# Kernel optimization log

Hardware: AMD Instinct MI355X
Metric: run time of the kernel (lower is better)

## Reference

```python
import jax, jax.numpy as jnp
import numpy as np

N = 20000       # num_nodes
B = 4           # batch
D = 32          # input_dim
OUT = 64        # output_dim
S = 2           # n_supports
E = 640000      # edges per support (avg degree 32)
MAX_STEP = 3
M = MAX_STEP * S + 1  # num_metrics = 7


def setup_inputs() -> dict:
    key = jax.random.key(0)
    k = jax.random.split(key, 6)
    inputs = jax.random.normal(k[0], (B, N, D), dtype=jnp.float32)
    edge_src = jax.random.randint(k[1], (S, E), 0, N, dtype=jnp.int32)
    edge_dst = jax.random.randint(k[2], (S, E), 0, N, dtype=jnp.int32)
    # ~1/deg scaled values so the diffusion recurrence stays numerically tame
    edge_vals = jax.random.uniform(k[3], (S, E), dtype=jnp.float32) / 32.0
    W = jax.random.normal(k[4], (OUT, D * M), dtype=jnp.float32) * 0.05
    bias = jnp.zeros((OUT,), dtype=jnp.float32)
    return dict(inputs=inputs, edge_vals=edge_vals, W=W, bias=bias,
                edge_src=edge_src, edge_dst=edge_dst)


def _spmm(vals, src, dst, x):
    # y[i] = sum_{edges (i<-j)} vals * x[j]  == support.mm(x) for COO support
    return jax.ops.segment_sum(vals[:, None] * x[src], dst, num_segments=N)


def reference(inputs, edge_vals, W, bias, edge_src, edge_dst):
    b, n, d = inputs.shape
    # x0: [N, D*B], batch fastest (matches permute([1,2,0]).reshape(n,-1))
    x0 = jnp.transpose(inputs, (1, 2, 0)).reshape(n, -1)
    xs = [x0]
    for s in range(S):
        v, sr, ds = edge_vals[s], edge_src[s], edge_dst[s]
        x1 = _spmm(v, sr, ds, x0)
        xs.append(x1)
        for _ in range(2, MAX_STEP + 1):
            x2 = 2.0 * _spmm(v, sr, ds, x1) - x0
            xs.append(x2)
            # NOTE: faithful to source aliasing quirk — x0 is mutated here,
            # so the next support starts from the mutated x0.
            x1, x0 = x2, x1
    x = jnp.stack(xs, 0)                       # [M, N, D*B]
    x = x.reshape(-1, n, d, b)                 # [M, N, D, B]
    x = jnp.transpose(x, (3, 1, 2, 0))         # [B, N, D, M]
    x = x.reshape(b, n, -1)                    # [B, N, D*M], M fastest
    return x @ W.T + bias                      # [B, N, OUT]
```

## Files before the change

### kernel.cpp

```cpp
#include <hip/hip_runtime.h>

#define N_NODES 20000
#define BATCH   4
#define DIN     32
#define DOUT    64
#define MSTEPS  7
#define ROW     128
#define NROW    896
#define NROWU   448
#define NT      79
#define KB2     (2 * NT)
#define CHUNK   2048
#define SLOT    12288
#define WSLOT   3584
#define RGRID   (N_NODES / 4)
#define PGRID   625
#define TGRID   1250

typedef short  short8 __attribute__((ext_vector_type(8)));
typedef float  f32x4  __attribute__((ext_vector_type(4)));

__device__ __forceinline__ unsigned short f2bf(float f) {
    unsigned u = __float_as_uint(f);
    unsigned r = u + 0x7fff + ((u >> 16) & 1);
    return (unsigned short)(r >> 16);
}
__device__ __forceinline__ float bf_lo(unsigned p) { return __uint_as_float(p << 16); }
__device__ __forceinline__ float bf_hi(unsigned p) { return __uint_as_float(p & 0xffff0000u); }

__global__ void init_k(int* __restrict__ cursor, const float* __restrict__ W,
                       unsigned short* __restrict__ Wbf) {
    if (blockIdx.x == 0) {
        if (threadIdx.x < KB2) cursor[threadIdx.x] = threadIdx.x * SLOT;
        return;
    }
    int i = (int)(blockIdx.x - 1) * 256 + threadIdx.x;
    int m = i >> 11;
    int o = (i >> 5) & 63;
    int c = i & 31;
    Wbf[i] = f2bf(W[o * 224 + c * 7 + m]);
}

__global__ void __launch_bounds__(256) p2t_k(const int* __restrict__ src,
                                             const int* __restrict__ dst,
                                             const float* __restrict__ vals,
                                             int* __restrict__ cursor,
                                             uint2* __restrict__ staged,
                                             const float* __restrict__ in,
                                             unsigned short* __restrict__ xs, int E) {
    __shared__ int lhist[KB2];
    __shared__ int lbase[KB2];
    __shared__ int gbase[KB2];
    __shared__ int sc[256];
    __shared__ uint2 buf[CHUNK];
    __shared__ unsigned short kk[CHUNK];
    int t = threadIdx.x;
    if (blockIdx.x >= PGRID) {
        int tid = (blockIdx.x - PGRID) * 256 + t;
        if (tid < N_NODES * 16) {
            int dq = tid & 3;
            int b  = (tid >> 2) & 3;
            int n  = tid >> 4;
            int d0 = dq * 8;
            const float* ip = in + ((size_t)b * N_NODES + n) * DIN + d0;
            float4 f0 = *(const float4*)ip;
            float4 f1 = *(const float4*)(ip + 4);
            uint4 o;
            o.x = (unsigned)f2bf(f0.x) | ((unsigned)f2bf(f0.y) << 16);
            o.y = (unsigned)f2bf(f0.z) | ((unsigned)f2bf(f0.w) << 16);
            o.z = (unsigned)f2bf(f1.x) | ((unsigned)f2bf(f1.y) << 16);
            o.w = (unsigned)f2bf(f1.z) | ((unsigned)f2bf(f1.w) << 16);
            *(uint4*)(xs + (size_t)n * NROW + b * 32 + d0) = o;
        }
        return;
    }
    int base = blockIdx.x * CHUNK;
    int nval = min(CHUNK, 2 * E - base);
    for (int i = t; i < KB2; i += 256) lhist[i] = 0;
    __syncthreads();
    int k[CHUNK / 256], pos[CHUNK / 256];
    uint2 pay[CHUNK / 256];
#pragma unroll
    for (int j = 0; j < CHUNK / 256; ++j) {
        int i = j * 256 + t;
        int e = base + i;
        if (i < nval) {
            int s = (e >= E) ? 1 : 0;
            int d = dst[e];
            pay[j] = make_uint2((unsigned)src[e] | ((unsigned)f2bf(vals[e]) << 16),
                                (unsigned)d);
            k[j] = s * NT + (d >> 8);
            pos[j] = atomicAdd(&lhist[k[j]], 1);
        } else k[j] = -1;
    }
    __syncthreads();
    int v = (t < KB2) ? lhist[t] : 0;
    sc[t] = v;
    __syncthreads();
    for (int off = 1; off < 256; off <<= 1) {
        int a = (t >= off) ? sc[t - off] : 0;
        __syncthreads();
        sc[t] += a;
        __syncthreads();
    }
    if (t < KB2) lbase[t] = sc[t] - v;
    __syncthreads();
    if (t < KB2 && lhist[t]) gbase[t] = atomicAdd(&cursor[t], lhist[t]);
#pragma unroll
    for (int j = 0; j < CHUNK / 256; ++j) {
        if (k[j] >= 0) {
            int slot = lbase[k[j]] + pos[j];
            buf[slot] = pay[j];
            kk[slot] = (unsigned short)k[j];
        }
    }
    __syncthreads();
#pragma unroll
    for (int j = 0; j < CHUNK / 256; ++j) {
        int i = j * 256 + t;
        if (i < nval) {
            int b = kk[i];
            staged[gbase[b] + (i - lbase[b])] = buf[i];
        }
    }
}

__global__ void __launch_bounds__(256) p3_fine_k(const uint2* __restrict__ staged,
                                                 const int* __restrict__ cursor,
                                                 int2* __restrict__ row_desc,
                                                 unsigned* __restrict__ csr) {
    __shared__ int lhist[64];
    __shared__ int sc[64];
    __shared__ int lcur[64];
    int bb = blockIdx.x;
    int b = bb >> 2, sub = bb & 3;
    int s = b / NT, tile = b - s * NT;
    int w0loc = sub * 64;
    int seg0 = b * SLOT;
    int len = cursor[b] - seg0;
    int t = threadIdx.x;
    if (t < 64) lhist[t] = 0;
    __syncthreads();
    for (int i = t; i < len; i += 256) {
        int dl = (int)(staged[seg0 + i].y & 255) - w0loc;
        if (dl >= 0 && dl < 64) atomicAdd(&lhist[dl], 1);
    }
    __syncthreads();
    int cntr = (t < 64) ? lhist[t] : 0;
    int pl = (cntr + 15) & ~15;
    if (t < 64) sc[t] = pl;
    __syncthreads();
    for (int off = 1; off < 64; off <<= 1) {
        int a = (t < 64 && t >= off) ? sc[t - off] : 0;
        __syncthreads();
        if (t < 64) sc[t] += a;
        __syncthreads();
    }
    int wbase = bb * WSLOT;
    if (t < 64) {
        int excl = sc[t] - pl;
        lcur[t] = wbase + excl;
        int nd = tile * 256 + w0loc + t;
        if (nd < N_NODES) row_desc[s * N_NODES + nd] = make_int2(wbase + excl, pl);
    }
    __syncthreads();
    for (int i = t; i < len; i += 256) {
        uint2 u = staged[seg0 + i];
        int dl = (int)(u.y & 255) - w0loc;
        if (dl >= 0 && dl < 64) {
            int p = atomicAdd(&lcur[dl], 1);
            csr[p] = u.x;
        }
    }
    if (t < 64) {
        int excl = sc[t] - pl;
        for (int i = cntr; i < pl; ++i) csr[wbase + excl + i] = 0u;
    }
}

__device__ __forceinline__ void issue8(const unsigned* __restrict__ csr, int e,
                                       const unsigned* __restrict__ xb, int lane,
                                       unsigned c[8], unsigned p[8]) {
    uint4 q0 = *(const uint4*)(csr + e);
    uint4 q1 = *(const uint4*)(csr + e + 4);
    c[0]=q0.x; c[1]=q0.y; c[2]=q0.z; c[3]=q0.w;
    c[4]=q1.x; c[5]=q1.y; c[6]=q1.z; c[7]=q1.w;
#pragma unroll
    for (int j = 0; j < 8; ++j)
        p[j] = xb[(size_t)(c[j] & 0xffffu) * NROWU + lane];
}

__device__ __forceinline__ void fmac8(const unsigned c[8], const unsigned p[8],
                                      float acc[8]) {
#pragma unroll
    for (int j = 0; j < 8; ++j) {
        float v = bf_hi(c[j]);
        acc[j & 3]       = fmaf(v, bf_lo(p[j]), acc[j & 3]);
        acc[4 + (j & 3)] = fmaf(v, bf_hi(p[j]), acc[4 + (j & 3)]);
    }
}

__device__ __forceinline__ void spmm_core(const int2* __restrict__ rdesc,
                                          const unsigned* __restrict__ csr,
                                          const unsigned* __restrict__ xb,
                                          const unsigned* __restrict__ xprevb,
                                          unsigned* __restrict__ yb,
                                          float alpha, int node, int lane) {
    int2 rd = rdesc[node];
    int start = rd.x, len = rd.y;
    float acc[8];
#pragma unroll
    for (int j = 0; j < 8; ++j) acc[j] = 0.f;
    if (len) {
        unsigned cA[8], pA[8], cB[8], pB[8];
        int n8 = len >> 3;
        issue8(csr, start, xb, lane, cA, pA);
        int k = 1;
        for (; k + 1 < n8; k += 2) {
            issue8(csr, start + k * 8, xb, lane, cB, pB);
            fmac8(cA, pA, acc);
            issue8(csr, start + (k + 1) * 8, xb, lane, cA, pA);
            fmac8(cB, pB, acc);
        }
        if (k < n8) {
            issue8(csr, start + k * 8, xb, lane, cB, pB);
            fmac8(cA, pA, acc);
            fmac8(cB, pB, acc);
        } else {
            fmac8(cA, pA, acc);
        }
    }
    float r0 = alpha * ((acc[0] + acc[1]) + (acc[2] + acc[3]));
    float r1 = alpha * ((acc[4] + acc[5]) + (acc[6] + acc[7]));
    if (xprevb) {
        unsigned pp = xprevb[(size_t)node * NROWU + lane];
        r0 -= bf_lo(pp);
        r1 -= bf_hi(pp);
    }
    yb[(size_t)node * NROWU + lane] = (unsigned)f2bf(r0) | ((unsigned)f2bf(r1) << 16);
}

__global__ void __launch_bounds__(256) spmm_row_k(const int2* __restrict__ rdesc,
                                                  const unsigned* __restrict__ csr,
                                                  const unsigned short* __restrict__ x,
                                                  const unsigned short* __restrict__ xprev,
                                                  unsigned short* __restrict__ y, float alpha) {
    int node = __builtin_amdgcn_readfirstlane(blockIdx.x * 4 + (threadIdx.x >> 6));
    int lane = threadIdx.x & 63;
    spmm_core(rdesc, csr, (const unsigned*)x, (const unsigned*)xprev, (unsigned*)y,
              alpha, node, lane);
}

__global__ void __launch_bounds__(256) spmm_dual_k(const int2* __restrict__ rdA,
                                                   const int2* __restrict__ rdB,
                                                   const unsigned* __restrict__ csr,
                                                   const unsigned short* __restrict__ x,
                                                   const unsigned short* __restrict__ xprevA,
                                                   unsigned short* __restrict__ yA,
                                                   unsigned short* __restrict__ yB) {
    int bid = blockIdx.x;
    int second = (bid >= RGRID) ? 1 : 0;
    int node = __builtin_amdgcn_readfirstlane((bid - second * RGRID) * 4 + (threadIdx.x >> 6));
    int lane = threadIdx.x & 63;
    const int2* rd = second ? rdB : rdA;
    const unsigned* xprevb = second ? nullptr : (const unsigned*)xprevA;
    unsigned* yb = second ? (unsigned*)yB : (unsigned*)yA;
    float alpha = second ? 1.0f : 2.0f;
    spmm_core(rd, csr, (const unsigned*)x, xprevb, yb, alpha, node, lane);
}

__global__ void __launch_bounds__(256) epilogue_mfma_k(const unsigned short* __restrict__ xs,
                                                       const unsigned short* __restrict__ Wbf,
                                                       const float* __restrict__ bias,
                                                       float* __restrict__ out) {
    int tid = threadIdx.x;
    int lane = tid & 63, ot = tid >> 6;
    int col = lane & 15, quad = lane >> 4;
    int o = ot * 16 + col;

    short8 bfrag[MSTEPS];
#pragma unroll
    for (int m = 0; m < MSTEPS; ++m)
        bfrag[m] = *(const short8*)&Wbf[m * 2048 + o * 32 + quad * 8];
    float bo = bias[o];

    int n0 = blockIdx.x * 16;
    const unsigned short* arow = xs + (size_t)(n0 + col) * NROW + quad * 8;

    f32x4 acc[BATCH];
#pragma unroll
    for (int b = 0; b < BATCH; ++b)
        acc[b] = (f32x4){bo, bo, bo, bo};

#pragma unroll
    for (int m = 0; m < MSTEPS; ++m) {
#pragma unroll
        for (int b = 0; b < BATCH; ++b) {
            short8 a = *(const short8*)&arow[m * 128 + b * 32];
            acc[b] = __builtin_amdgcn_mfma_f32_16x16x32_bf16(a, bfrag[m], acc[b], 0, 0, 0);
        }
    }

#pragma unroll
    for (int b = 0; b < BATCH; ++b) {
#pragma unroll
        for (int reg = 0; reg < 4; ++reg) {
            int n = n0 + quad * 4 + reg;
            out[((size_t)b * N_NODES + n) * DOUT + o] = acc[b][reg];
        }
    }
}

extern "C" void kernel_launch(void* const* d_in, const int* in_sizes, int n_in,
                              void* d_out, int out_size, void* d_ws, size_t ws_size,
                              hipStream_t stream) {
    const float* inputs    = (const float*)d_in[0];
    const float* edge_vals = (const float*)d_in[1];
    const float* W         = (const float*)d_in[2];
    const float* bias      = (const float*)d_in[3];
    const int*   edge_src  = (const int*)d_in[4];
    const int*   edge_dst  = (const int*)d_in[5];
    float* out = (float*)d_out;
    const int E = in_sizes[1] / 2;

    unsigned short* xs = (unsigned short*)d_ws;
    uint2* staged  = (uint2*)(xs + (size_t)N_NODES * NROW);
    unsigned* csr  = (unsigned*)(staged + (size_t)KB2 * SLOT);
    int* cursor    = (int*)(csr + (size_t)4 * KB2 * WSLOT);
    int2* row_desc = (int2*)(cursor + KB2 + 2);
    unsigned short* Wbf = (unsigned short*)(row_desc + 2 * N_NODES);

    const int epgrid = N_NODES / 16;

    init_k<<<57, 256, 0, stream>>>(cursor, W, Wbf);
    p2t_k<<<PGRID + TGRID, 256, 0, stream>>>(edge_src, edge_dst, edge_vals, cursor,
                                             staged, inputs, xs, E);
    p3_fine_k<<<4 * KB2, 256, 0, stream>>>(staged, cursor, row_desc, csr);

    const int2* rd0 = row_desc;
    const int2* rd1 = row_desc + N_NODES;

    unsigned short* X0 = xs + 0 * ROW;
    unsigned short* X1 = xs + 1 * ROW;
    unsigned short* X2 = xs + 2 * ROW;
    unsigned short* X3 = xs + 3 * ROW;
    unsigned short* X4 = xs + 4 * ROW;
    unsigned short* X5 = xs + 5 * ROW;
    unsigned short* X6 = xs + 6 * ROW;

    spmm_row_k<<<RGRID, 256, 0, stream>>>(rd0, csr, X0, nullptr, X1, 1.0f);
    spmm_row_k<<<RGRID, 256, 0, stream>>>(rd0, csr, X1, X0,      X2, 2.0f);
    spmm_dual_k<<<2 * RGRID, 256, 0, stream>>>(rd0, rd1, csr, X2, X1, X3, X4);
    spmm_row_k<<<RGRID, 256, 0, stream>>>(rd1, csr, X4, X2, X5, 2.0f);
    spmm_row_k<<<RGRID, 256, 0, stream>>>(rd1, csr, X5, X4, X6, 2.0f);

    epilogue_mfma_k<<<epgrid, 256, 0, stream>>>(xs, Wbf, bias, out);
}
```

Before: 238.5 us.

## Fuse final diffusion SpMMs into epilogue and widen gather batches to 16

```diff
diff --git a/kernel.cpp b/kernel.cpp
--- a/kernel.cpp
+++ b/kernel.cpp
@@ -8,6 +8,7 @@
 #define ROW     128
 #define NROW    896
 #define NROWU   448
+#define PLN     656
 #define NT      79
 #define KB2     (2 * NT)
 #define CHUNK   2048
@@ -178,6 +179,32 @@
     }
 }
 
+__device__ __forceinline__ void issue16(const unsigned* __restrict__ csr, int e,
+                                        const unsigned* __restrict__ xb, int lane,
+                                        unsigned c[16], unsigned p[16]) {
+    uint4 q0 = *(const uint4*)(csr + e);
+    uint4 q1 = *(const uint4*)(csr + e + 4);
+    uint4 q2 = *(const uint4*)(csr + e + 8);
+    uint4 q3 = *(const uint4*)(csr + e + 12);
+    c[0]=q0.x;  c[1]=q0.y;  c[2]=q0.z;  c[3]=q0.w;
+    c[4]=q1.x;  c[5]=q1.y;  c[6]=q1.z;  c[7]=q1.w;
+    c[8]=q2.x;  c[9]=q2.y;  c[10]=q2.z; c[11]=q2.w;
+    c[12]=q3.x; c[13]=q3.y; c[14]=q3.z; c[15]=q3.w;
+#pragma unroll
+    for (int j = 0; j < 16; ++j)
+        p[j] = xb[(size_t)(c[j] & 0xffffu) * NROWU + lane];
+}
+
+__device__ __forceinline__ void fmac16(const unsigned c[16], const unsigned p[16],
+                                       float acc[8]) {
+#pragma unroll
+    for (int j = 0; j < 16; ++j) {
+        float v = bf_hi(c[j]);
+        acc[j & 3]       = fmaf(v, bf_lo(p[j]), acc[j & 3]);
+        acc[4 + (j & 3)] = fmaf(v, bf_hi(p[j]), acc[4 + (j & 3)]);
+    }
+}
+
 __device__ __forceinline__ void issue8(const unsigned* __restrict__ csr, int e,
                                        const unsigned* __restrict__ xb, int lane,
                                        unsigned c[8], unsigned p[8]) {
@@ -208,6 +235,43 @@
                                           float alpha, int node, int lane) {
     int2 rd = rdesc[node];
     int start = rd.x, len = rd.y;
+    float acc[8];
+#pragma unroll
+    for (int j = 0; j < 8; ++j) acc[j] = 0.f;
+    if (len) {
+        unsigned cA[16], pA[16], cB[16], pB[16];
+        int n16 = len >> 4;
+        issue16(csr, start, xb, lane, cA, pA);
+        int k = 1;
+        for (; k + 1 < n16; k += 2) {
+            issue16(csr, start + k * 16, xb, lane, cB, pB);
+            fmac16(cA, pA, acc);
+            issue16(csr, start + (k + 1) * 16, xb, lane, cA, pA);
+            fmac16(cB, pB, acc);
+        }
+        if (k < n16) {
+            issue16(csr, start + k * 16, xb, lane, cB, pB);
+            fmac16(cA, pA, acc);
+            fmac16(cB, pB, acc);
+        } else {
+            fmac16(cA, pA, acc);
+        }
+    }
+    float r0 = alpha * ((acc[0] + acc[1]) + (acc[2] + acc[3]));
+    float r1 = alpha * ((acc[4] + acc[5]) + (acc[6] + acc[7]));
+    if (xprevb) {
+        unsigned pp = xprevb[(size_t)node * NROWU + lane];
+        r0 -= bf_lo(pp);
+        r1 -= bf_hi(pp);
+    }
+    yb[(size_t)node * NROWU + lane] = (unsigned)f2bf(r0) | ((unsigned)f2bf(r1) << 16);
+}
+
+__device__ __forceinline__ unsigned gather_pack8(const unsigned* __restrict__ csr,
+                                                 int start, int len,
+                                                 const unsigned* __restrict__ xb,
+                                                 const unsigned* __restrict__ xprevb,
+                                                 float alpha, int node, int lane) {
     float acc[8];
 #pragma unroll
     for (int j = 0; j < 8; ++j) acc[j] = 0.f;
@@ -237,7 +301,7 @@
         r0 -= bf_lo(pp);
         r1 -= bf_hi(pp);
     }
-    yb[(size_t)node * NROWU + lane] = (unsigned)f2bf(r0) | ((unsigned)f2bf(r1) << 16);
+    return (unsigned)f2bf(r0) | ((unsigned)f2bf(r1) << 16);
 }
 
 __global__ void __launch_bounds__(256) spmm_row_k(const int2* __restrict__ rdesc,
@@ -251,28 +315,14 @@
               alpha, node, lane);
 }
 
-__global__ void __launch_bounds__(256) spmm_dual_k(const int2* __restrict__ rdA,
-                                                   const int2* __restrict__ rdB,
-                                                   const unsigned* __restrict__ csr,
-                                                   const unsigned short* __restrict__ x,
-                                                   const unsigned short* __restrict__ xprevA,
-                                                   unsigned short* __restrict__ yA,
-                                                   unsigned short* __restrict__ yB) {
-    int bid = blockIdx.x;
-    int second = (bid >= RGRID) ? 1 : 0;
-    int node = __builtin_amdgcn_readfirstlane((bid - second * RGRID) * 4 + (threadIdx.x >> 6));
-    int lane = threadIdx.x & 63;
-    const int2* rd = second ? rdB : rdA;
-    const unsigned* xprevb = second ? nullptr : (const unsigned*)xprevA;
-    unsigned* yb = second ? (unsigned*)yB : (unsigned*)yA;
-    float alpha = second ? 1.0f : 2.0f;
-    spmm_core(rd, csr, (const unsigned*)x, xprevb, yb, alpha, node, lane);
-}
-
 __global__ void __launch_bounds__(256) epilogue_mfma_k(const unsigned short* __restrict__ xs,
                                                        const unsigned short* __restrict__ Wbf,
                                                        const float* __restrict__ bias,
-                                                       float* __restrict__ out) {
+                                                       float* __restrict__ out,
+                                                       const int2* __restrict__ rd0,
+                                                       const int2* __restrict__ rd1,
+                                                       const unsigned* __restrict__ csr) {
+    __shared__ unsigned short Alds[28 * PLN];
     int tid = threadIdx.x;
     int lane = tid & 63, ot = tid >> 6;
     int col = lane & 15, quad = lane >> 4;
@@ -285,7 +335,39 @@
     float bo = bias[o];
 
     int n0 = blockIdx.x * 16;
-    const unsigned short* arow = xs + (size_t)(n0 + col) * NROW + quad * 8;
+
+#pragma unroll
+    for (int it = 0; it < 5; ++it) {
+        int idx = tid + it * 256;
+        int r   = idx / 80;
+        int rem = idx - r * 80;
+        int si  = rem >> 4;
+        int m   = si + (si >= 3 ? 1 : 0);
+        int b   = (rem >> 2) & 3;
+        int d0  = (rem & 3) * 8;
+        uint4 q = *(const uint4*)(xs + (size_t)(n0 + r) * NROW + m * 128 + b * 32 + d0);
+        *(uint4*)&Alds[(b * 7 + m) * PLN + r * 40 + d0] = q;
+    }
+
+    {
+        const unsigned* xb = (const unsigned*)xs;
+        int lb = lane >> 4;
+        int ld = (lane & 15) * 2;
+#pragma unroll
+        for (int i = 0; i < 4; ++i) {
+            int rr = ot * 4 + i;
+            int nn = __builtin_amdgcn_readfirstlane(n0 + rr);
+            int2 r3 = rd0[nn];
+            unsigned v3 = gather_pack8(csr, r3.x, r3.y, xb + 2 * 64, xb + 1 * 64,
+                                       2.0f, nn, lane);
+            *(unsigned*)&Alds[(lb * 7 + 3) * PLN + rr * 40 + ld] = v3;
+            int2 r6 = rd1[nn];
+            unsigned v6 = gather_pack8(csr, r6.x, r6.y, xb + 5 * 64, xb + 4 * 64,
+                                       2.0f, nn, lane);
+            *(unsigned*)&Alds[(lb * 7 + 6) * PLN + rr * 40 + ld] = v6;
+        }
+    }
+    __syncthreads();
 
     f32x4 acc[BATCH];
 #pragma unroll
@@ -296,7 +378,7 @@
     for (int m = 0; m < MSTEPS; ++m) {
 #pragma unroll
         for (int b = 0; b < BATCH; ++b) {
-            short8 a = *(const short8*)&arow[m * 128 + b * 32];
+            short8 a = *(const short8*)&Alds[(b * 7 + m) * PLN + col * 40 + quad * 8];
             acc[b] = __builtin_amdgcn_mfma_f32_16x16x32_bf16(a, bfrag[m], acc[b], 0, 0, 0);
         }
     }
@@ -343,16 +425,13 @@
     unsigned short* X0 = xs + 0 * ROW;
     unsigned short* X1 = xs + 1 * ROW;
     unsigned short* X2 = xs + 2 * ROW;
-    unsigned short* X3 = xs + 3 * ROW;
     unsigned short* X4 = xs + 4 * ROW;
     unsigned short* X5 = xs + 5 * ROW;
-    unsigned short* X6 = xs + 6 * ROW;
 
     spmm_row_k<<<RGRID, 256, 0, stream>>>(rd0, csr, X0, nullptr, X1, 1.0f);
     spmm_row_k<<<RGRID, 256, 0, stream>>>(rd0, csr, X1, X0,      X2, 2.0f);
-    spmm_dual_k<<<2 * RGRID, 256, 0, stream>>>(rd0, rd1, csr, X2, X1, X3, X4);
-    spmm_row_k<<<RGRID, 256, 0, stream>>>(rd1, csr, X4, X2, X5, 2.0f);
-    spmm_row_k<<<RGRID, 256, 0, stream>>>(rd1, csr, X5, X4, X6, 2.0f);
-
-    epilogue_mfma_k<<<epgrid, 256, 0, stream>>>(xs, Wbf, bias, out);
-}
+    spmm_row_k<<<RGRID, 256, 0, stream>>>(rd1, csr, X2, nullptr, X4, 1.0f);
+    spmm_row_k<<<RGRID, 256, 0, stream>>>(rd1, csr, X4, X2,      X5, 2.0f);
+
+    epilogue_mfma_k<<<epgrid, 256, 0, stream>>>(xs, Wbf, bias, out, rd0, rd1, csr);
+}
```

Measured after the change: 235.7 us. No clear change (-1.2%).
